# Kernel optimization log

Hardware: AMD Instinct MI355X
Metric: run time of the kernel (lower is better)

The kernel has to match this reference:

```python
import jax, jax.numpy as jnp
import numpy as np
import math

EMBED_DIM = 512
NUM_HEADS = 8
BLOCK_SIZE = 16
RANK = 32
B, N = 1, 4096
HEAD_DIM = EMBED_DIM // NUM_HEADS
SCALE = math.sqrt(HEAD_DIM)  # note: the torch module MULTIPLIES q by sqrt(head_dim)


def _block_causal_mask(n, block):
    # block-diagonal lower-triangular mask, identical for every head
    idx = jnp.arange(n)
    same_block = (idx[:, None] // block) == (idx[None, :] // block)
    causal = idx[:, None] >= idx[None, :]
    return (same_block & causal).astype(jnp.float32)  # [N, N]


def setup_inputs() -> dict:
    key = jax.random.key(0)
    ks = jax.random.split(key, 12)
    s = 0.02
    C, R = EMBED_DIM, RANK
    return {
        "x": jax.random.normal(ks[0], (B, N, C), dtype=jnp.float32),
        # low-rank query proj: Linear(C->R) then Linear(R->C); torch weight is [out, in]
        "q_w1": jax.random.normal(ks[1], (R, C), dtype=jnp.float32) * s,
        "q_w2": jax.random.normal(ks[2], (C, R), dtype=jnp.float32) * s,
        # key_value: Linear(C->2R) then Linear(2R->2C)
        "kv_w1": jax.random.normal(ks[3], (2 * R, C), dtype=jnp.float32) * s,
        "kv_w2": jax.random.normal(ks[4], (2 * C, 2 * R), dtype=jnp.float32) * s,
        # dynamic_focus: depthwise 1x1 conv (per-channel scale+bias) then pointwise 1x1 conv
        "dw_w": jax.random.normal(ks[5], (C,), dtype=jnp.float32) * s,
        "dw_b": jax.random.normal(ks[6], (C,), dtype=jnp.float32) * s,
        "pw_w": jax.random.normal(ks[7], (C, C), dtype=jnp.float32) * s,
        "pw_b": jax.random.normal(ks[8], (C,), dtype=jnp.float32) * s,
        # output proj: Linear(C->R) then Linear(R->C)
        "p_w1": jax.random.normal(ks[9], (R, C), dtype=jnp.float32) * s,
        "p_w2": jax.random.normal(ks[10], (C, R), dtype=jnp.float32) * s,
    }


def reference(x, q_w1, q_w2, kv_w1, kv_w2, dw_w, dw_b, pw_w, pw_b, p_w1, p_w2):
    Bv, Nv, C = x.shape
    H, D = NUM_HEADS, HEAD_DIM

    # low-rank q / kv projections (no bias)
    q = (x @ q_w1.T) @ q_w2.T                              # [B, N, C]
    kv = (x @ kv_w1.T) @ kv_w2.T                           # [B, N, 2C]

    q = q.reshape(Bv, Nv, H, D).transpose(0, 2, 1, 3)      # [B, H, N, D]
    kv = kv.reshape(Bv, Nv, 2, H, D).transpose(2, 0, 3, 1, 4)
    k, v = kv[0], kv[1]                                    # [B, H, N, D]

    q = q * SCALE
    attn = jnp.einsum("bhnd,bhmd->bhnm", q, k)             # [B, H, N, N]
    # faithful to source: full-row softmax FIRST, then block-diag causal mask
    mask = _block_causal_mask(Nv, BLOCK_SIZE)              # [N, N]
    attn = jax.nn.softmax(attn, axis=-1) * mask

    wv = jnp.einsum("bhnm,bhmd->bhnd", attn, v)            # [B, H, N, D]
    wv = wv.transpose(0, 2, 1, 3).reshape(Bv, Nv, C)       # [B, N, C]

    # dynamic_focus: depthwise 1x1 conv == per-channel affine; pointwise 1x1 conv == linear.
    # Spatial reshape to (sqrt(N), sqrt(N)) is a no-op for 1x1 convs, so stay in [B, N, C].
    dyn = wv * dw_w + dw_b
    dyn = dyn @ pw_w.T + pw_b

    y = dyn + x
    y = (y @ p_w1.T) @ p_w2.T
    return y
```

## Files before the change

### kernel.cpp

```cpp
#include <hip/hip_runtime.h>

#define NFULL 4096
#define CDIM  512
#define HEADS 8
#define DDIM  64

typedef unsigned short u16;
typedef short bf16x8 __attribute__((ext_vector_type(8)));
typedef float f32x4 __attribute__((ext_vector_type(4)));

#if __has_builtin(__builtin_amdgcn_exp2f)
__device__ __forceinline__ float exp2_hw(float x) { return __builtin_amdgcn_exp2f(x); }
#else
__device__ __forceinline__ float exp2_hw(float x) {
  float r;
  asm volatile("v_exp_f32 %0, %1\n\ts_nop 1" : "=v"(r) : "v"(x));
  return r;
}
#endif
#define EXP2(x) exp2_hw(x)

#define QSCALE 11.541560327111707f

__device__ __forceinline__ float dot4(float4 a, float4 b) {
  return a.x * b.x + a.y * b.y + a.z * b.z + a.w * b.w;
}

__device__ __forceinline__ u16 f2bf(float x) {
  union { float f; unsigned u; } v; v.f = x;
  unsigned r = v.u + 0x7fffu + ((v.u >> 16) & 1u);
  return (u16)(r >> 16);
}

__global__ __launch_bounds__(256) void k_pre(const float* __restrict__ x,
                                             const float* __restrict__ qw1,
                                             const float* __restrict__ kvw1,
                                             u16* __restrict__ t_bf,
                                             const float* __restrict__ pww,
                                             const float* __restrict__ dww,
                                             const float* __restrict__ dwb,
                                             const float* __restrict__ pwb,
                                             float* __restrict__ bias2,
                                             u16* __restrict__ pwbf) {
  __shared__ __align__(16) u16 Xs[64][72];
  __shared__ __align__(16) u16 Ws[96][72];
  const int tid = threadIdx.x;
  if (blockIdx.x >= 64) {
    const int b = blockIdx.x - 64;
    if (b < 2) {
      const int c = b * 256 + tid;
      float acc = 0.f;
      for (int e = 0; e < 512; e += 4)
        acc += dot4(*(const float4*)&pww[(size_t)c * 512 + e], *(const float4*)&dwb[e]);
      bias2[c] = acc + pwb[c];
    } else {
      const int base = (b - 2) * 4096 + tid * 16;
      const int e0 = base & 511;
      u16 o[16];
#pragma unroll
      for (int q = 0; q < 4; ++q) {
        const float4 w = *(const float4*)&pww[base + q * 4];
        const float4 d = *(const float4*)&dww[e0 + q * 4];
        o[q * 4 + 0] = f2bf(w.x * d.x); o[q * 4 + 1] = f2bf(w.y * d.y);
        o[q * 4 + 2] = f2bf(w.z * d.z); o[q * 4 + 3] = f2bf(w.w * d.w);
      }
      *(uint4*)&pwbf[base] = *(const uint4*)&o[0];
      *(uint4*)&pwbf[base + 8] = *(const uint4*)&o[8];
    }
    return;
  }

  const int r0 = blockIdx.x * 64;
  const int wave = tid >> 6, lane = tid & 63;
  const int lrow = lane & 15, g = lane >> 4;

  f32x4 acc[6];
#pragma unroll
  for (int sub = 0; sub < 6; ++sub) acc[sub] = (f32x4){0.f, 0.f, 0.f, 0.f};

  for (int k0 = 0; k0 < 512; k0 += 64) {
    __syncthreads();
    {
      const int row = tid >> 2, c16 = (tid & 3) * 16;
      const float* __restrict__ src = x + (size_t)(r0 + row) * 512 + k0 + c16;
      u16 tmp[16];
#pragma unroll
      for (int q = 0; q < 4; ++q) {
        const float4 v = *(const float4*)(src + q * 4);
        tmp[q * 4 + 0] = f2bf(v.x); tmp[q * 4 + 1] = f2bf(v.y);
        tmp[q * 4 + 2] = f2bf(v.z); tmp[q * 4 + 3] = f2bf(v.w);
      }
      *(uint4*)&Xs[row][c16] = *(const uint4*)&tmp[0];
      *(uint4*)&Xs[row][c16 + 8] = *(const uint4*)&tmp[8];
    }
    for (int u = tid; u < 384; u += 256) {
      const int c = u >> 2, c16 = (u & 3) * 16;
      const float* __restrict__ src =
          (c < 32 ? qw1 + (size_t)c * 512 : kvw1 + (size_t)(c - 32) * 512) + k0 + c16;
      u16 tmp[16];
#pragma unroll
      for (int q = 0; q < 4; ++q) {
        const float4 v = *(const float4*)(src + q * 4);
        tmp[q * 4 + 0] = f2bf(v.x); tmp[q * 4 + 1] = f2bf(v.y);
        tmp[q * 4 + 2] = f2bf(v.z); tmp[q * 4 + 3] = f2bf(v.w);
      }
      *(uint4*)&Ws[c][c16] = *(const uint4*)&tmp[0];
      *(uint4*)&Ws[c][c16 + 8] = *(const uint4*)&tmp[8];
    }
    __syncthreads();
    const bf16x8 a0 = *(const bf16x8*)&Xs[wave * 16 + lrow][g * 8];
    const bf16x8 a1 = *(const bf16x8*)&Xs[wave * 16 + lrow][32 + g * 8];
#pragma unroll
    for (int sub = 0; sub < 6; ++sub) {
      const bf16x8 b0 = *(const bf16x8*)&Ws[sub * 16 + lrow][g * 8];
      const bf16x8 b1 = *(const bf16x8*)&Ws[sub * 16 + lrow][32 + g * 8];
      acc[sub] = __builtin_amdgcn_mfma_f32_16x16x32_bf16(a0, b0, acc[sub], 0, 0, 0);
      acc[sub] = __builtin_amdgcn_mfma_f32_16x16x32_bf16(a1, b1, acc[sub], 0, 0, 0);
    }
  }
#pragma unroll
  for (int sub = 0; sub < 6; ++sub)
#pragma unroll
    for (int j = 0; j < 4; ++j)
      t_bf[(size_t)(r0 + wave * 16 + g * 4 + j) * 96 + sub * 16 + lrow] = f2bf(acc[sub][j]);
}

__global__ __launch_bounds__(256) void k_proj2(const u16* __restrict__ t_bf,
                                               const float* __restrict__ qw2,
                                               const float* __restrict__ kvw2,
                                               u16* __restrict__ qb,
                                               u16* __restrict__ kb,
                                               float* __restrict__ vh) {
  __shared__ __align__(16) u16 Ts[64][72];
  __shared__ __align__(16) u16 Wsh[128][72];
  const int cb = blockIdx.x % 12;
  const int r0 = (blockIdx.x / 12) * 64;
  const int tid = threadIdx.x;
  const int wave = tid >> 6, lane = tid & 63;
  const int lrow = lane & 15, g = lane >> 4;
  const bool isq = cb < 4;
  const int c0 = isq ? cb * 128 : 512 + (cb - 4) * 128;

  for (int u = tid; u < 512; u += 256) {
    const int row = u >> 3, ch = (u & 7) * 8;
    uint4 v = {0u, 0u, 0u, 0u};
    if (isq) {
      if (ch < 32) v = *(const uint4*)&t_bf[(size_t)(r0 + row) * 96 + ch];
    } else {
      v = *(const uint4*)&t_bf[(size_t)(r0 + row) * 96 + 32 + ch];
    }
    *(uint4*)&Ts[row][ch] = v;
  }
  if (isq) {
    for (int u = tid; u < 1024; u += 256) {
      const int col = u >> 3, cf = (u & 7) * 4;
      const float4 v = *(const float4*)&qw2[(size_t)(c0 + col) * 32 + cf];
      u16 tmp[4] = {f2bf(v.x), f2bf(v.y), f2bf(v.z), f2bf(v.w)};
      *(uint2*)&Wsh[col][cf] = *(const uint2*)&tmp[0];
    }
    for (int u = tid; u < 512; u += 256) {
      const int col = u >> 2, ch = 32 + (u & 3) * 8;
      const uint4 z = {0u, 0u, 0u, 0u};
      *(uint4*)&Wsh[col][ch] = z;
    }
  } else {
    for (int u = tid; u < 2048; u += 256) {
      const int col = u >> 4, cf = (u & 15) * 4;
      const float4 v = *(const float4*)&kvw2[(size_t)(c0 - 512 + col) * 64 + cf];
      u16 tmp[4] = {f2bf(v.x), f2bf(v.y), f2bf(v.z), f2bf(v.w)};
      *(uint2*)&Wsh[col][cf] = *(const uint2*)&tmp[0];
    }
  }
  __syncthreads();

  const bf16x8 a0 = *(const bf16x8*)&Ts[wave * 16 + lrow][g * 8];
  const bf16x8 a1 = *(const bf16x8*)&Ts[wave * 16 + lrow][32 + g * 8];
#pragma unroll
  for (int sub = 0; sub < 8; ++sub) {
    const bf16x8 b0 = *(const bf16x8*)&Wsh[sub * 16 + lrow][g * 8];
    const bf16x8 b1 = *(const bf16x8*)&Wsh[sub * 16 + lrow][32 + g * 8];
    f32x4 acc = {0.f, 0.f, 0.f, 0.f};
    acc = __builtin_amdgcn_mfma_f32_16x16x32_bf16(a0, b0, acc, 0, 0, 0);
    acc = __builtin_amdgcn_mfma_f32_16x16x32_bf16(a1, b1, acc, 0, 0, 0);
    const int colg = c0 + sub * 16 + lrow;
#pragma unroll
    for (int j = 0; j < 4; ++j) {
      const int n = r0 + wave * 16 + g * 4 + j;
      if (colg < 512) {
        qb[((size_t)(colg >> 6) * NFULL + n) * 64 + (colg & 63)] = f2bf(acc[j] * QSCALE);
      } else if (colg < 1024) {
        const int c2 = colg - 512;
        kb[((size_t)(c2 >> 6) * NFULL + n) * 64 + (c2 & 63)] = f2bf(acc[j]);
      } else {
        const int c2 = colg - 1024;
        vh[((size_t)(c2 >> 6) * NFULL + n) * 64 + (c2 & 63)] = acc[j];
      }
    }
  }
}

__global__ __launch_bounds__(256, 4) void k_attn(const u16* __restrict__ qb,
                                                 const u16* __restrict__ kb,
                                                 const float* __restrict__ vh,
                                                 float* __restrict__ wv,
                                                 float* __restrict__ dsp) {
  __shared__ __align__(16) u16 KB[4][64][64];
  __shared__ float P_lds[4][16][17];
  __shared__ float Ds[4][4][16];

  const int h = blockIdx.x & 7;
  const int qt = (blockIdx.x >> 3) & 63;
  const int s = blockIdx.x >> 9;
  const int q0 = qt * 64;
  const int tid = threadIdx.x;
  const int wave = tid >> 6, lane = tid & 63;
  const int lrow = lane & 15, g = lane >> 4;

  const u16* __restrict__ Qg = qb + ((size_t)h * NFULL + q0) * 64;
  const u16* __restrict__ Kg = kb + ((size_t)h * NFULL + (size_t)s * 2048) * 64;

  bf16x8 qf[4][2];
#pragma unroll
  for (int f = 0; f < 4; ++f) {
    qf[f][0] = *(const bf16x8*)&Qg[(f * 16 + lrow) * 64 + g * 8];
    qf[f][1] = *(const bf16x8*)&Qg[(f * 16 + lrow) * 64 + 32 + g * 8];
  }

  const int srow8 = lane >> 3;
  const int scol = ((lane & 7) ^ srow8) << 3;

#define STAGE(T, B)                                                           \
  do {                                                                        \
    const u16* tb_ = Kg + (size_t)(T) * 64 * 64;                              \
    {                                                                         \
      const u16* src_ = tb_ + (wave * 16 + srow8) * 64 + scol;                \
      u16* dst_ = &KB[(B)][wave * 16][0];                                     \
      __builtin_amdgcn_global_load_lds(                                       \
          (const __attribute__((address_space(1))) unsigned*)src_,            \
          (__attribute__((address_space(3))) unsigned*)dst_, 16, 0, 0);       \
    }                                                                         \
    {                                                                         \
      const u16* src_ = tb_ + (wave * 16 + 8 + srow8) * 64 + scol;            \
      u16* dst_ = &KB[(B)][wave * 16][0] + 512;                               \
      __builtin_amdgcn_global_load_lds(                                       \
          (const __attribute__((address_space(1))) unsigned*)src_,            \
          (__attribute__((address_space(3))) unsigned*)dst_, 16, 0, 0);       \
    }                                                                         \
  } while (0)

  const int rsw = wave * 16 + lrow;
  const int x0 = (g ^ (lrow & 7)) * 8;
  const int x1 = ((g + 4) ^ (lrow & 7)) * 8;

  float dsum[4] = {0.f, 0.f, 0.f, 0.f};
  const bool dg = (s == (qt >> 5));
  const int tdiag = qt & 31;

  STAGE(0, 0); STAGE(1, 1); STAGE(2, 2);

  for (int t = 0; t < 32; ++t) {
    const int b = t & 3;
    if (t + 3 < 32) STAGE(t + 3, (t + 3) & 3);
    if (t < 29)       asm volatile("s_waitcnt vmcnt(6)" ::: "memory");
    else if (t == 29) asm volatile("s_waitcnt vmcnt(4)" ::: "memory");
    else if (t == 30) asm volatile("s_waitcnt vmcnt(2)" ::: "memory");
    else              asm volatile("s_waitcnt vmcnt(0)" ::: "memory");

    const bf16x8 kf0 = *(const bf16x8*)&KB[b][rsw][x0];
    const bf16x8 kf1 = *(const bf16x8*)&KB[b][rsw][x1];
    f32x4 a[4];
    __builtin_amdgcn_s_setprio(1);
#pragma unroll
    for (int f = 0; f < 4; ++f) {
      f32x4 t4 = {0.f, 0.f, 0.f, 0.f};
      t4 = __builtin_amdgcn_mfma_f32_16x16x32_bf16(kf0, qf[f][0], t4, 0, 0, 0);
      t4 = __builtin_amdgcn_mfma_f32_16x16x32_bf16(kf1, qf[f][1], t4, 0, 0, 0);
      a[f] = t4;
    }
    __builtin_amdgcn_s_setprio(0);
    const bool isd = dg && (t == tdiag);
#pragma unroll
    for (int f = 0; f < 4; ++f) {
      const float e0 = EXP2(a[f][0]);
      const float e1 = EXP2(a[f][1]);
      const float e2 = EXP2(a[f][2]);
      const float e3 = EXP2(a[f][3]);
      dsum[f] += (e0 + e1) + (e2 + e3);
      if (isd && f == wave) {
        const int rr = g * 4;
        P_lds[wave][rr + 0][lrow] = (rr + 0 <= lrow) ? e0 : 0.f;
        P_lds[wave][rr + 1][lrow] = (rr + 1 <= lrow) ? e1 : 0.f;
        P_lds[wave][rr + 2][lrow] = (rr + 2 <= lrow) ? e2 : 0.f;
        P_lds[wave][rr + 3][lrow] = (rr + 3 <= lrow) ? e3 : 0.f;
      }
    }
  }
#undef STAGE

#pragma unroll
  for (int f = 0; f < 4; ++f) {
    dsum[f] += __shfl_xor(dsum[f], 16);
    dsum[f] += __shfl_xor(dsum[f], 32);
  }
  if (g == 0) {
#pragma unroll
    for (int f = 0; f < 4; ++f) Ds[wave][f][lrow] = dsum[f];
  }
  __syncthreads();

  if (tid < 64) {
    const int f = tid >> 4, r = tid & 15;
    const float den = Ds[0][f][r] + Ds[1][f][r] + Ds[2][f][r] + Ds[3][f][r];
    dsp[((size_t)s * HEADS + h) * NFULL + q0 + f * 16 + r] = den;
  }

  if (dg) {
    const float* __restrict__ V =
        vh + ((size_t)h * NFULL + q0 + wave * 16) * 64 + g * 16;
    float o[16];
#pragma unroll
    for (int dd = 0; dd < 16; ++dd) o[dd] = 0.f;
#pragma unroll
    for (int k = 0; k < 16; ++k) {
      const float p = P_lds[wave][k][lrow];
      const float4 v0 = *(const float4*)&V[k * 64 + 0];
      const float4 v1 = *(const float4*)&V[k * 64 + 4];
      const float4 v2 = *(const float4*)&V[k * 64 + 8];
      const float4 v3 = *(const float4*)&V[k * 64 + 12];
      o[0] += p * v0.x;  o[1] += p * v0.y;  o[2] += p * v0.z;  o[3] += p * v0.w;
      o[4] += p * v1.x;  o[5] += p * v1.y;  o[6] += p * v1.z;  o[7] += p * v1.w;
      o[8] += p * v2.x;  o[9] += p * v2.y;  o[10] += p * v2.z; o[11] += p * v2.w;
      o[12] += p * v3.x; o[13] += p * v3.y; o[14] += p * v3.z; o[15] += p * v3.w;
    }
    float* __restrict__ op =
        wv + (size_t)(q0 + wave * 16 + lrow) * CDIM + h * 64 + g * 16;
#pragma unroll
    for (int c4 = 0; c4 < 4; ++c4) {
      float4 r;
      r.x = o[c4 * 4 + 0]; r.y = o[c4 * 4 + 1];
      r.z = o[c4 * 4 + 2]; r.w = o[c4 * 4 + 3];
      *(float4*)&op[c4 * 4] = r;
    }
  }
}

__global__ __launch_bounds__(256) void k_dyn(const float* __restrict__ wv,
                                             const float* __restrict__ x,
                                             const u16* __restrict__ pwbf,
                                             const float* __restrict__ bias2,
                                             const float* __restrict__ dsp,
                                             float* __restrict__ y) {
  __shared__ __align__(16) u16 Ab[64][72];
  __shared__ __align__(16) u16 Wb[64][72];
  const int rb = blockIdx.x >> 3, cb = blockIdx.x & 7;
  const int r0 = rb * 64, c0 = cb * 64;
  const int tid = threadIdx.x;
  const int wave = tid >> 6, lane = tid & 63;
  const int lrow = lane & 15, g = lane >> 4;
  const int srow = tid >> 2;
  const int skc = (tid & 3) * 16;

  float inv8[8];
#pragma unroll
  for (int hh = 0; hh < 8; ++hh) {
    const size_t base = (size_t)hh * NFULL + r0 + srow;
    inv8[hh] = 1.0f / (dsp[base] + dsp[(size_t)8 * NFULL + base]);
  }

  f32x4 acc[4];
#pragma unroll
  for (int ct = 0; ct < 4; ++ct) acc[ct] = (f32x4){0.f, 0.f, 0.f, 0.f};

  const float* __restrict__ ap = wv + (size_t)(r0 + srow) * 512 + skc;
  const u16* __restrict__ wp = pwbf + (size_t)(c0 + srow) * 512 + skc;
  float4 a4[4];
#pragma unroll
  for (int e = 0; e < 4; ++e) a4[e] = *(const float4*)(ap + e * 4);
  uint4 w0 = *(const uint4*)wp;
  uint4 w1 = *(const uint4*)(wp + 8);

  for (int k0 = 0; k0 < 512; k0 += 64) {
    const float sc = inv8[k0 >> 6];
    u16 ab16[16];
#pragma unroll
    for (int e = 0; e < 4; ++e) {
      ab16[e * 4 + 0] = f2bf(a4[e].x * sc);
      ab16[e * 4 + 1] = f2bf(a4[e].y * sc);
      ab16[e * 4 + 2] = f2bf(a4[e].z * sc);
      ab16[e * 4 + 3] = f2bf(a4[e].w * sc);
    }
    __syncthreads();
    *(uint4*)&Ab[srow][skc] = *(const uint4*)&ab16[0];
    *(uint4*)&Ab[srow][skc + 8] = *(const uint4*)&ab16[8];
    *(uint4*)&Wb[srow][skc] = w0;
    *(uint4*)&Wb[srow][skc + 8] = w1;
    __syncthreads();
    if (k0 + 64 < 512) {
#pragma unroll
      for (int e = 0; e < 4; ++e) a4[e] = *(const float4*)(ap + k0 + 64 + e * 4);
      w0 = *(const uint4*)(wp + k0 + 64);
      w1 = *(const uint4*)(wp + k0 + 64 + 8);
    }
#pragma unroll
    for (int kk = 0; kk < 2; ++kk) {
      const bf16x8 af = *(const bf16x8*)&Ab[wave * 16 + lrow][kk * 32 + g * 8];
#pragma unroll
      for (int ct = 0; ct < 4; ++ct) {
        const bf16x8 wf = *(const bf16x8*)&Wb[ct * 16 + lrow][kk * 32 + g * 8];
        acc[ct] = __builtin_amdgcn_mfma_f32_16x16x32_bf16(wf, af, acc[ct], 0, 0, 0);
      }
    }
  }
  const int row = r0 + wave * 16 + lrow;
#pragma unroll
  for (int ct = 0; ct < 4; ++ct) {
    const int c = c0 + ct * 16 + g * 4;
    const float4 bb = *(const float4*)&bias2[c];
    const float4 xv = *(const float4*)&x[(size_t)row * 512 + c];
    float4 res;
    res.x = acc[ct][0] + bb.x + xv.x;
    res.y = acc[ct][1] + bb.y + xv.y;
    res.z = acc[ct][2] + bb.z + xv.z;
    res.w = acc[ct][3] + bb.w + xv.w;
    *(float4*)&y[(size_t)row * 512 + c] = res;
  }
}

__global__ __launch_bounds__(256) void k_pout(const float* __restrict__ y,
                                              const float* __restrict__ pw1,
                                              const float* __restrict__ pw2,
                                              float* __restrict__ out) {
  __shared__ __align__(16) u16 yb[16][520];
  __shared__ float tp_part[2][32][17];
  const int r0 = blockIdx.x * 16;
  const int tid = threadIdx.x;
  const int wave = tid >> 6, lane = tid & 63;
  const int lrow = lane & 15, g = lane >> 4;

  for (int rep = 0; rep < 8; ++rep) {
    const int l = rep * 256 + tid;
    const int row = l >> 7, c4 = (l & 127) << 2;
    const float4 v = *(const float4*)&y[(size_t)(r0 + row) * 512 + c4];
    yb[row][c4 + 0] = f2bf(v.x); yb[row][c4 + 1] = f2bf(v.y);
    yb[row][c4 + 2] = f2bf(v.z); yb[row][c4 + 3] = f2bf(v.w);
  }
  __syncthreads();

  {
    const int ct1 = wave & 1, kh = wave >> 1;
    f32x4 acc = {0.f, 0.f, 0.f, 0.f};
#pragma unroll
    for (int ks = 0; ks < 8; ++ks) {
      const int K = kh * 256 + ks * 32 + g * 8;
      union { u16 a[8]; bf16x8 v; } aw;
      const float4 wv0 = *(const float4*)&pw1[(size_t)(ct1 * 16 + lrow) * 512 + K];
      const float4 wv1 = *(const float4*)&pw1[(size_t)(ct1 * 16 + lrow) * 512 + K + 4];
      aw.a[0] = f2bf(wv0.x); aw.a[1] = f2bf(wv0.y);
      aw.a[2] = f2bf(wv0.z); aw.a[3] = f2bf(wv0.w);
      aw.a[4] = f2bf(wv1.x); aw.a[5] = f2bf(wv1.y);
      aw.a[6] = f2bf(wv1.z); aw.a[7] = f2bf(wv1.w);
      const bf16x8 bf = *(const bf16x8*)&yb[lrow][K];
      acc = __builtin_amdgcn_mfma_f32_16x16x32_bf16(aw.v, bf, acc, 0, 0, 0);
    }
#pragma unroll
    for (int j = 0; j < 4; ++j)
      tp_part[kh][ct1 * 16 + g * 4 + j][lrow] = acc[j];
  }
  __syncthreads();

  union { u16 a[8]; bf16x8 v; } bq;
#pragma unroll
  for (int i = 0; i < 8; ++i) {
    const int k = g * 8 + i;
    bq.a[i] = f2bf(tp_part[0][k][lrow] + tp_part[1][k][lrow]);
  }

#pragma unroll
  for (int t = 0; t < 8; ++t) {
    const int ct = wave * 8 + t;
    union { u16 a[8]; bf16x8 v; } aw;
    const float4 wv0 = *(const float4*)&pw2[(size_t)(ct * 16 + lrow) * 32 + g * 8];
    const float4 wv1 = *(const float4*)&pw2[(size_t)(ct * 16 + lrow) * 32 + g * 8 + 4];
    aw.a[0] = f2bf(wv0.x); aw.a[1] = f2bf(wv0.y);
    aw.a[2] = f2bf(wv0.z); aw.a[3] = f2bf(wv0.w);
    aw.a[4] = f2bf(wv1.x); aw.a[5] = f2bf(wv1.y);
    aw.a[6] = f2bf(wv1.z); aw.a[7] = f2bf(wv1.w);
    f32x4 acc = {0.f, 0.f, 0.f, 0.f};
    acc = __builtin_amdgcn_mfma_f32_16x16x32_bf16(aw.v, bq.v, acc, 0, 0, 0);
    float4 res;
    res.x = acc[0]; res.y = acc[1]; res.z = acc[2]; res.w = acc[3];
    *(float4*)&out[(size_t)(r0 + lrow) * 512 + ct * 16 + g * 4] = res;
  }
}

extern "C" void kernel_launch(void* const* d_in, const int* in_sizes, int n_in,
                              void* d_out, int out_size, void* d_ws, size_t ws_size,
                              hipStream_t stream) {
  const float* x     = (const float*)d_in[0];
  const float* q_w1  = (const float*)d_in[1];
  const float* q_w2  = (const float*)d_in[2];
  const float* kv_w1 = (const float*)d_in[3];
  const float* kv_w2 = (const float*)d_in[4];
  const float* dw_w  = (const float*)d_in[5];
  const float* dw_b  = (const float*)d_in[6];
  const float* pw_w  = (const float*)d_in[7];
  const float* pw_b  = (const float*)d_in[8];
  const float* p_w1  = (const float*)d_in[9];
  const float* p_w2  = (const float*)d_in[10];
  float* out = (float*)d_out;

  char* ws = (char*)d_ws;
  u16*   t_bf  = (u16*)ws;
  float* dsp   = (float*)ws;
  float* bias2 = (float*)(ws + 786432);
  u16*   pwbf  = (u16*)(ws + 786432 + 4096);
  u16*   qbw   = pwbf + 262144;
  u16*   kbw   = qbw + (size_t)HEADS * NFULL * DDIM;
  float* y     = (float*)qbw;
  float* vh    = (float*)(kbw + (size_t)HEADS * NFULL * DDIM);
  float* wvf   = vh + (size_t)HEADS * NFULL * DDIM;

  k_pre<<<130, 256, 0, stream>>>(x, q_w1, kv_w1, t_bf, pw_w, dw_w, dw_b, pw_b,
                                 bias2, pwbf);
  k_proj2<<<(NFULL / 64) * 12, 256, 0, stream>>>(t_bf, q_w2, kv_w2, qbw, kbw, vh);
  k_attn<<<2 * HEADS * (NFULL / 64), 256, 0, stream>>>(qbw, kbw, vh, wvf, dsp);
  k_dyn<<<(NFULL / 64) * 8, 256, 0, stream>>>(wvf, x, pwbf, bias2, dsp, y);
  k_pout<<<NFULL / 16, 256, 0, stream>>>(y, p_w1, p_w2, out);
}
```

Before: 88.98 us.

## Fuse low-rank projection kernels, unroll attention pipeline, store residual in bf16

Merges the two low-rank projection kernels into one. Each block now keeps the rank-96 intermediate in shared memory and produces half of the 12 output column groups, so the t_bf round-trip through global memory and one launch go away. The attention K/V staging loop is restructured into a lambda with a manually unrolled two-tile steady state and an explicit tail, which removes the per-iteration waitcnt branching. The intermediate y between k_dyn and k_pout is now stored as bf16 instead of fp32, halving that traffic; the fused projection redoes the first-stage GEMM in both halves and launches fewer blocks than the old second-stage kernel.

```diff
diff --git a/kernel.cpp b/kernel.cpp
--- a/kernel.cpp
+++ b/kernel.cpp
@@ -32,21 +32,26 @@
   return (u16)(r >> 16);
 }
 
-__global__ __launch_bounds__(256) void k_pre(const float* __restrict__ x,
-                                             const float* __restrict__ qw1,
-                                             const float* __restrict__ kvw1,
-                                             u16* __restrict__ t_bf,
-                                             const float* __restrict__ pww,
-                                             const float* __restrict__ dww,
-                                             const float* __restrict__ dwb,
-                                             const float* __restrict__ pwb,
-                                             float* __restrict__ bias2,
-                                             u16* __restrict__ pwbf) {
-  __shared__ __align__(16) u16 Xs[64][72];
-  __shared__ __align__(16) u16 Ws[96][72];
+__global__ __launch_bounds__(256) void k_proj(const float* __restrict__ x,
+                                              const float* __restrict__ qw1,
+                                              const float* __restrict__ kvw1,
+                                              const float* __restrict__ qw2,
+                                              const float* __restrict__ kvw2,
+                                              const float* __restrict__ pww,
+                                              const float* __restrict__ dww,
+                                              const float* __restrict__ dwb,
+                                              const float* __restrict__ pwb,
+                                              u16* __restrict__ qb,
+                                              u16* __restrict__ kb,
+                                              float* __restrict__ vh,
+                                              float* __restrict__ bias2,
+                                              u16* __restrict__ pwbf) {
+  __shared__ __align__(16) u16 buf[11520];
+  __shared__ __align__(16) u16 Ts[64][104];
   const int tid = threadIdx.x;
-  if (blockIdx.x >= 64) {
-    const int b = blockIdx.x - 64;
+
+  if (blockIdx.x >= 128) {
+    const int b = blockIdx.x - 128;
     if (b < 2) {
       const int c = b * 256 + tid;
       float acc = 0.f;
@@ -70,9 +75,13 @@
     return;
   }
 
-  const int r0 = blockIdx.x * 64;
+  const int rb = blockIdx.x >> 1, half = blockIdx.x & 1;
+  const int r0 = rb * 64;
   const int wave = tid >> 6, lane = tid & 63;
   const int lrow = lane & 15, g = lane >> 4;
+
+  u16 (*Xs)[72] = (u16(*)[72])buf;
+  u16 (*Ws)[72] = (u16(*)[72])(buf + 64 * 72);
 
   f32x4 acc[6];
 #pragma unroll
@@ -108,92 +117,75 @@
       *(uint4*)&Ws[c][c16 + 8] = *(const uint4*)&tmp[8];
     }
     __syncthreads();
-    const bf16x8 a0 = *(const bf16x8*)&Xs[wave * 16 + lrow][g * 8];
-    const bf16x8 a1 = *(const bf16x8*)&Xs[wave * 16 + lrow][32 + g * 8];
+    const bf16x8 xa0 = *(const bf16x8*)&Xs[wave * 16 + lrow][g * 8];
+    const bf16x8 xa1 = *(const bf16x8*)&Xs[wave * 16 + lrow][32 + g * 8];
 #pragma unroll
     for (int sub = 0; sub < 6; ++sub) {
       const bf16x8 b0 = *(const bf16x8*)&Ws[sub * 16 + lrow][g * 8];
       const bf16x8 b1 = *(const bf16x8*)&Ws[sub * 16 + lrow][32 + g * 8];
-      acc[sub] = __builtin_amdgcn_mfma_f32_16x16x32_bf16(a0, b0, acc[sub], 0, 0, 0);
-      acc[sub] = __builtin_amdgcn_mfma_f32_16x16x32_bf16(a1, b1, acc[sub], 0, 0, 0);
-    }
-  }
+      acc[sub] = __builtin_amdgcn_mfma_f32_16x16x32_bf16(xa0, b0, acc[sub], 0, 0, 0);
+      acc[sub] = __builtin_amdgcn_mfma_f32_16x16x32_bf16(xa1, b1, acc[sub], 0, 0, 0);
+    }
+  }
+  __syncthreads();
 #pragma unroll
   for (int sub = 0; sub < 6; ++sub)
 #pragma unroll
     for (int j = 0; j < 4; ++j)
-      t_bf[(size_t)(r0 + wave * 16 + g * 4 + j) * 96 + sub * 16 + lrow] = f2bf(acc[sub][j]);
-}
-
-__global__ __launch_bounds__(256) void k_proj2(const u16* __restrict__ t_bf,
-                                               const float* __restrict__ qw2,
-                                               const float* __restrict__ kvw2,
-                                               u16* __restrict__ qb,
-                                               u16* __restrict__ kb,
-                                               float* __restrict__ vh) {
-  __shared__ __align__(16) u16 Ts[64][72];
-  __shared__ __align__(16) u16 Wsh[128][72];
-  const int cb = blockIdx.x % 12;
-  const int r0 = (blockIdx.x / 12) * 64;
-  const int tid = threadIdx.x;
-  const int wave = tid >> 6, lane = tid & 63;
-  const int lrow = lane & 15, g = lane >> 4;
-  const bool isq = cb < 4;
-  const int c0 = isq ? cb * 128 : 512 + (cb - 4) * 128;
-
-  for (int u = tid; u < 512; u += 256) {
-    const int row = u >> 3, ch = (u & 7) * 8;
-    uint4 v = {0u, 0u, 0u, 0u};
+      Ts[wave * 16 + g * 4 + j][sub * 16 + lrow] = f2bf(acc[sub][j]);
+  __syncthreads();
+
+  const bf16x8 aq = *(const bf16x8*)&Ts[wave * 16 + lrow][g * 8];
+  const bf16x8 a0 = *(const bf16x8*)&Ts[wave * 16 + lrow][32 + g * 8];
+  const bf16x8 a1 = *(const bf16x8*)&Ts[wave * 16 + lrow][64 + g * 8];
+  u16 (*Wsh)[72] = (u16(*)[72])buf;
+
+  for (int i = 0; i < 6; ++i) {
+    const int cb = half * 6 + i;
+    const bool isq = cb < 4;
+    const int c0 = isq ? cb * 128 : 512 + (cb - 4) * 128;
+    __syncthreads();
     if (isq) {
-      if (ch < 32) v = *(const uint4*)&t_bf[(size_t)(r0 + row) * 96 + ch];
+      for (int u = tid; u < 1024; u += 256) {
+        const int col = u >> 3, cf = (u & 7) * 4;
+        const float4 v = *(const float4*)&qw2[(size_t)(c0 + col) * 32 + cf];
+        u16 tmp[4] = {f2bf(v.x), f2bf(v.y), f2bf(v.z), f2bf(v.w)};
+        *(uint2*)&Wsh[col][cf] = *(const uint2*)&tmp[0];
+      }
     } else {
-      v = *(const uint4*)&t_bf[(size_t)(r0 + row) * 96 + 32 + ch];
-    }
-    *(uint4*)&Ts[row][ch] = v;
-  }
-  if (isq) {
-    for (int u = tid; u < 1024; u += 256) {
-      const int col = u >> 3, cf = (u & 7) * 4;
-      const float4 v = *(const float4*)&qw2[(size_t)(c0 + col) * 32 + cf];
-      u16 tmp[4] = {f2bf(v.x), f2bf(v.y), f2bf(v.z), f2bf(v.w)};
-      *(uint2*)&Wsh[col][cf] = *(const uint2*)&tmp[0];
-    }
-    for (int u = tid; u < 512; u += 256) {
-      const int col = u >> 2, ch = 32 + (u & 3) * 8;
-      const uint4 z = {0u, 0u, 0u, 0u};
-      *(uint4*)&Wsh[col][ch] = z;
-    }
-  } else {
-    for (int u = tid; u < 2048; u += 256) {
-      const int col = u >> 4, cf = (u & 15) * 4;
-      const float4 v = *(const float4*)&kvw2[(size_t)(c0 - 512 + col) * 64 + cf];
-      u16 tmp[4] = {f2bf(v.x), f2bf(v.y), f2bf(v.z), f2bf(v.w)};
-      *(uint2*)&Wsh[col][cf] = *(const uint2*)&tmp[0];
-    }
-  }
-  __syncthreads();
-
-  const bf16x8 a0 = *(const bf16x8*)&Ts[wave * 16 + lrow][g * 8];
-  const bf16x8 a1 = *(const bf16x8*)&Ts[wave * 16 + lrow][32 + g * 8];
-#pragma unroll
-  for (int sub = 0; sub < 8; ++sub) {
-    const bf16x8 b0 = *(const bf16x8*)&Wsh[sub * 16 + lrow][g * 8];
-    const bf16x8 b1 = *(const bf16x8*)&Wsh[sub * 16 + lrow][32 + g * 8];
-    f32x4 acc = {0.f, 0.f, 0.f, 0.f};
-    acc = __builtin_amdgcn_mfma_f32_16x16x32_bf16(a0, b0, acc, 0, 0, 0);
-    acc = __builtin_amdgcn_mfma_f32_16x16x32_bf16(a1, b1, acc, 0, 0, 0);
-    const int colg = c0 + sub * 16 + lrow;
-#pragma unroll
-    for (int j = 0; j < 4; ++j) {
-      const int n = r0 + wave * 16 + g * 4 + j;
-      if (colg < 512) {
-        qb[((size_t)(colg >> 6) * NFULL + n) * 64 + (colg & 63)] = f2bf(acc[j] * QSCALE);
-      } else if (colg < 1024) {
-        const int c2 = colg - 512;
-        kb[((size_t)(c2 >> 6) * NFULL + n) * 64 + (c2 & 63)] = f2bf(acc[j]);
+      for (int u = tid; u < 2048; u += 256) {
+        const int col = u >> 4, cf = (u & 15) * 4;
+        const float4 v = *(const float4*)&kvw2[(size_t)(c0 - 512 + col) * 64 + cf];
+        u16 tmp[4] = {f2bf(v.x), f2bf(v.y), f2bf(v.z), f2bf(v.w)};
+        *(uint2*)&Wsh[col][cf] = *(const uint2*)&tmp[0];
+      }
+    }
+    __syncthreads();
+#pragma unroll
+    for (int sub = 0; sub < 8; ++sub) {
+      f32x4 a2 = {0.f, 0.f, 0.f, 0.f};
+      if (isq) {
+        const bf16x8 b0 = *(const bf16x8*)&Wsh[sub * 16 + lrow][g * 8];
+        a2 = __builtin_amdgcn_mfma_f32_16x16x32_bf16(aq, b0, a2, 0, 0, 0);
       } else {
-        const int c2 = colg - 1024;
-        vh[((size_t)(c2 >> 6) * NFULL + n) * 64 + (c2 & 63)] = acc[j];
+        const bf16x8 b0 = *(const bf16x8*)&Wsh[sub * 16 + lrow][g * 8];
+        const bf16x8 b1 = *(const bf16x8*)&Wsh[sub * 16 + lrow][32 + g * 8];
+        a2 = __builtin_amdgcn_mfma_f32_16x16x32_bf16(a0, b0, a2, 0, 0, 0);
+        a2 = __builtin_amdgcn_mfma_f32_16x16x32_bf16(a1, b1, a2, 0, 0, 0);
+      }
+      const int colg = c0 + sub * 16 + lrow;
+#pragma unroll
+      for (int j = 0; j < 4; ++j) {
+        const int n = r0 + wave * 16 + g * 4 + j;
+        if (colg < 512) {
+          qb[((size_t)(colg >> 6) * NFULL + n) * 64 + (colg & 63)] = f2bf(a2[j] * QSCALE);
+        } else if (colg < 1024) {
+          const int c2 = colg - 512;
+          kb[((size_t)(c2 >> 6) * NFULL + n) * 64 + (c2 & 63)] = f2bf(a2[j]);
+        } else {
+          const int c2 = colg - 1024;
+          vh[((size_t)(c2 >> 6) * NFULL + n) * 64 + (c2 & 63)] = a2[j];
+        }
       }
     }
   }
@@ -256,16 +248,7 @@
   const bool dg = (s == (qt >> 5));
   const int tdiag = qt & 31;
 
-  STAGE(0, 0); STAGE(1, 1); STAGE(2, 2);
-
-  for (int t = 0; t < 32; ++t) {
-    const int b = t & 3;
-    if (t + 3 < 32) STAGE(t + 3, (t + 3) & 3);
-    if (t < 29)       asm volatile("s_waitcnt vmcnt(6)" ::: "memory");
-    else if (t == 29) asm volatile("s_waitcnt vmcnt(4)" ::: "memory");
-    else if (t == 30) asm volatile("s_waitcnt vmcnt(2)" ::: "memory");
-    else              asm volatile("s_waitcnt vmcnt(0)" ::: "memory");
-
+  auto tile = [&](int t, int b) {
     const bf16x8 kf0 = *(const bf16x8*)&KB[b][rsw][x0];
     const bf16x8 kf1 = *(const bf16x8*)&KB[b][rsw][x1];
     f32x4 a[4];
@@ -294,7 +277,27 @@
         P_lds[wave][rr + 3][lrow] = (rr + 3 <= lrow) ? e3 : 0.f;
       }
     }
-  }
+  };
+
+  STAGE(0, 0); STAGE(1, 1); STAGE(2, 2);
+
+  for (int t = 0; t < 28; t += 2) {
+    STAGE(t + 3, (t + 3) & 3);
+    asm volatile("s_waitcnt vmcnt(6)" ::: "memory");
+    tile(t, t & 3);
+    STAGE(t + 4, (t + 4) & 3);
+    asm volatile("s_waitcnt vmcnt(6)" ::: "memory");
+    tile(t + 1, (t + 1) & 3);
+  }
+  STAGE(31, 3);
+  asm volatile("s_waitcnt vmcnt(6)" ::: "memory");
+  tile(28, 0);
+  asm volatile("s_waitcnt vmcnt(4)" ::: "memory");
+  tile(29, 1);
+  asm volatile("s_waitcnt vmcnt(2)" ::: "memory");
+  tile(30, 2);
+  asm volatile("s_waitcnt vmcnt(0)" ::: "memory");
+  tile(31, 3);
 #undef STAGE
 
 #pragma unroll
@@ -349,7 +352,7 @@
                                              const u16* __restrict__ pwbf,
                                              const float* __restrict__ bias2,
                                              const float* __restrict__ dsp,
-                                             float* __restrict__ y) {
+                                             u16* __restrict__ y16) {
   __shared__ __align__(16) u16 Ab[64][72];
   __shared__ __align__(16) u16 Wb[64][72];
   const int rb = blockIdx.x >> 3, cb = blockIdx.x & 7;
@@ -417,16 +420,16 @@
     const int c = c0 + ct * 16 + g * 4;
     const float4 bb = *(const float4*)&bias2[c];
     const float4 xv = *(const float4*)&x[(size_t)row * 512 + c];
-    float4 res;
-    res.x = acc[ct][0] + bb.x + xv.x;
-    res.y = acc[ct][1] + bb.y + xv.y;
-    res.z = acc[ct][2] + bb.z + xv.z;
-    res.w = acc[ct][3] + bb.w + xv.w;
-    *(float4*)&y[(size_t)row * 512 + c] = res;
-  }
-}
-
-__global__ __launch_bounds__(256) void k_pout(const float* __restrict__ y,
+    u16 o4[4];
+    o4[0] = f2bf(acc[ct][0] + bb.x + xv.x);
+    o4[1] = f2bf(acc[ct][1] + bb.y + xv.y);
+    o4[2] = f2bf(acc[ct][2] + bb.z + xv.z);
+    o4[3] = f2bf(acc[ct][3] + bb.w + xv.w);
+    *(uint2*)&y16[(size_t)row * 512 + c] = *(const uint2*)o4;
+  }
+}
+
+__global__ __launch_bounds__(256) void k_pout(const u16* __restrict__ y16,
                                               const float* __restrict__ pw1,
                                               const float* __restrict__ pw2,
                                               float* __restrict__ out) {
@@ -437,12 +440,10 @@
   const int wave = tid >> 6, lane = tid & 63;
   const int lrow = lane & 15, g = lane >> 4;
 
-  for (int rep = 0; rep < 8; ++rep) {
-    const int l = rep * 256 + tid;
-    const int row = l >> 7, c4 = (l & 127) << 2;
-    const float4 v = *(const float4*)&y[(size_t)(r0 + row) * 512 + c4];
-    yb[row][c4 + 0] = f2bf(v.x); yb[row][c4 + 1] = f2bf(v.y);
-    yb[row][c4 + 2] = f2bf(v.z); yb[row][c4 + 3] = f2bf(v.w);
+  for (int rep = 0; rep < 4; ++rep) {
+    const int idx = rep * 256 + tid;
+    const int row = idx >> 6, c8 = (idx & 63) * 8;
+    *(uint4*)&yb[row][c8] = *(const uint4*)&y16[(size_t)(r0 + row) * 512 + c8];
   }
   __syncthreads();
 
@@ -510,20 +511,18 @@
   float* out = (float*)d_out;
 
   char* ws = (char*)d_ws;
-  u16*   t_bf  = (u16*)ws;
   float* dsp   = (float*)ws;
   float* bias2 = (float*)(ws + 786432);
   u16*   pwbf  = (u16*)(ws + 786432 + 4096);
   u16*   qbw   = pwbf + 262144;
   u16*   kbw   = qbw + (size_t)HEADS * NFULL * DDIM;
-  float* y     = (float*)qbw;
+  u16*   y16   = qbw;
   float* vh    = (float*)(kbw + (size_t)HEADS * NFULL * DDIM);
   float* wvf   = vh + (size_t)HEADS * NFULL * DDIM;
 
-  k_pre<<<130, 256, 0, stream>>>(x, q_w1, kv_w1, t_bf, pw_w, dw_w, dw_b, pw_b,
-                                 bias2, pwbf);
-  k_proj2<<<(NFULL / 64) * 12, 256, 0, stream>>>(t_bf, q_w2, kv_w2, qbw, kbw, vh);
+  k_proj<<<194, 256, 0, stream>>>(x, q_w1, kv_w1, q_w2, kv_w2, pw_w, dw_w, dw_b,
+                                  pw_b, qbw, kbw, vh, bias2, pwbf);
   k_attn<<<2 * HEADS * (NFULL / 64), 256, 0, stream>>>(qbw, kbw, vh, wvf, dsp);
-  k_dyn<<<(NFULL / 64) * 8, 256, 0, stream>>>(wvf, x, pwbf, bias2, dsp, y);
-  k_pout<<<NFULL / 16, 256, 0, stream>>>(y, p_w1, p_w2, out);
-}
+  k_dyn<<<(NFULL / 64) * 8, 256, 0, stream>>>(wvf, x, pwbf, bias2, dsp, y16);
+  k_pout<<<NFULL / 16, 256, 0, stream>>>(y16, p_w1, p_w2, out);
+}
```

New measurement: 105.6 us. 18.7% more time.
